# Kernel optimization log

Hardware: AMD Instinct MI355X
Metric: run time of the kernel (lower is better)

Reference implementation:

```python
import jax, jax.numpy as jnp
import numpy as np

B, T, P, D = 8, 512, 2048, 768
TOKEN_HALF = 0.15
PATCH_HALF = 0.03  # small patch boxes


def _make_boxes(key, b, n, half):
    c = jax.random.uniform(key, (b, n, 2), dtype=jnp.float32)
    lo = jnp.clip(c - half, 0.0, 1.0)
    hi = jnp.clip(c + half, 0.0, 1.0)
    return jnp.concatenate([lo, hi], axis=-1)  # (b, n, 4): x0,y0,x1,y1


def setup_inputs() -> dict:
    key = jax.random.key(0)
    k1, k2, k3, k4 = jax.random.split(key, 4)
    patch_feats = jax.random.normal(k1, (B, P, D), dtype=jnp.float32)
    token_boxes = _make_boxes(k2, B, T, TOKEN_HALF)
    patch_boxes = _make_boxes(k3, B, P, PATCH_HALF)
    token_mask = jnp.ones((B, T), dtype=bool)
    scorer_w = jax.random.normal(k4, (D,), dtype=jnp.float32) * 0.02
    scorer_b = jnp.zeros((1,), dtype=jnp.float32)
    return {"patch_feats": patch_feats, "token_boxes": token_boxes,
            "patch_boxes": patch_boxes, "token_mask": token_mask,
            "scorer_w": scorer_w, "scorer_b": scorer_b}


def _patches_in_token_boxes(patch_boxes, tb):
    # patch center containment test: (B,T,P) bool
    cx = 0.5 * (patch_boxes[..., 0] + patch_boxes[..., 2])  # (B,P)
    cy = 0.5 * (patch_boxes[..., 1] + patch_boxes[..., 3])  # (B,P)
    cx = cx[:, None, :]
    cy = cy[:, None, :]
    return ((cx >= tb[..., 0:1]) & (cx <= tb[..., 2:3]) &
            (cy >= tb[..., 1:2]) & (cy <= tb[..., 3:4]))


def reference(patch_feats, token_boxes, patch_boxes, token_mask, scorer_w, scorer_b):
    # normalize token boxes if given in 0..1000 coords (data-dependent, via where)
    tb = token_boxes
    scale = jnp.where(tb.max() > 1.5, jnp.float32(1.0 / 1000.0), jnp.float32(1.0))
    tb = tb * scale

    in_box = _patches_in_token_boxes(patch_boxes, tb)          # (B,T,P)
    in_box = in_box & token_mask[:, :, None]
    region_mask = jnp.any(in_box, axis=-1)                      # (B,T)

    scores = patch_feats @ scorer_w + scorer_b[0]               # (B,P)
    scores = jnp.broadcast_to(scores[:, None, :], in_box.shape)  # (B,T,P)
    scores = jnp.where(in_box, scores, jnp.float32(-10000.0))
    attn = jax.nn.softmax(scores, axis=-1)                      # (B,T,P)

    region_feats = jnp.einsum('btp,bpd->btd', attn, patch_feats)
    region_feats = region_feats * region_mask[..., None].astype(region_feats.dtype)
    return region_feats, region_mask
```

## Files before the change

### kernel.cpp

```cpp
#include <hip/hip_runtime.h>

#define B 8
#define T 512
#define P 2048
#define D 768
#define KDIM P

typedef unsigned short ushort_t;
using short8 = __attribute__((ext_vector_type(8))) short;
using f32x4v = __attribute__((ext_vector_type(4))) float;

#define IDX_SCALE 0
#define IDX_SCORES 64
#define IDX_SCORES2 (64 + B*P)
#define IDX_CX (64 + B*P)
#define IDX_CY (64 + 2*B*P)
#define OFF_ATTN_BYTES 197120
#define OFF_FT_BYTES (OFF_ATTN_BYTES + (size_t)B*T*P*2)
#define WS_NEED (OFF_FT_BYTES + (size_t)B*D*P*2)

#define GLD16(gsrc, ldst) \
    __builtin_amdgcn_global_load_lds((const __attribute__((address_space(1))) void*)(gsrc), \
                                     (__attribute__((address_space(3))) void*)(ldst), 16, 0, 0)

#define SCHED_FENCE() __builtin_amdgcn_sched_barrier(0)
#define RAW_BARRIER() do { SCHED_FENCE(); __builtin_amdgcn_s_barrier(); SCHED_FENCE(); } while (0)

__device__ inline ushort_t f2bf(float x) {
    union { float f; unsigned u; } v; v.f = x;
    unsigned r = v.u + 0x7fffu + ((v.u >> 16) & 1u);
    return (ushort_t)(r >> 16);
}

__global__ void k_scale(const float* __restrict__ tboxes, float* __restrict__ ws) {
    __shared__ float red[4];
    int tid = threadIdx.x;
    float m = -1e30f;
    const float4* tb4 = (const float4*)tboxes;
    #pragma unroll
    for (int i = 0; i < 16; ++i) {
        float4 v = tb4[tid + i * 256];
        m = fmaxf(fmaxf(fmaxf(m, v.x), fmaxf(v.y, v.z)), v.w);
    }
    #pragma unroll
    for (int off = 1; off < 64; off <<= 1) m = fmaxf(m, __shfl_xor(m, off));
    if ((tid & 63) == 0) red[tid >> 6] = m;
    __syncthreads();
    if (tid == 0) {
        float mb = fmaxf(fmaxf(red[0], red[1]), fmaxf(red[2], red[3]));
        ws[IDX_SCALE] = (mb > 1.5f) ? (1.0f / 1000.0f) : 1.0f;
    }
}

__global__ __launch_bounds__(256) void k_prep(const float* __restrict__ feats,
        const float* __restrict__ w, float* __restrict__ ws, ushort_t* __restrict__ fT) {
    __shared__ float tile[2][64][65];
    __shared__ float sred[64][17];
    const int t = threadIdx.x;
    const int p0 = blockIdx.x * 64;
    const int z = blockIdx.y;
    const int b = blockIdx.z;
    const float4* f4 = (const float4*)(feats + ((size_t)b * P + p0) * D);
    const float4* w4 = (const float4*)w;
    const int tr = t >> 4, tc = t & 15;
    float sp[4] = {0.f, 0.f, 0.f, 0.f};

    float4 v[4];
    {
        int dt = z * 6;
        #pragma unroll
        for (int i = 0; i < 4; ++i)
            v[i] = f4[(size_t)(tr + 16 * i) * 192 + dt * 16 + tc];
    }
    int cur = 0;
    for (int it = 0; it < 6; ++it) {
        const int dt = z * 6 + it;
        float4 wv = w4[dt * 16 + tc];
        #pragma unroll
        for (int i = 0; i < 4; ++i) {
            int pr = tr + 16 * i;
            sp[i] += v[i].x * wv.x + v[i].y * wv.y + v[i].z * wv.z + v[i].w * wv.w;
            tile[cur][pr][tc * 4 + 0] = v[i].x;
            tile[cur][pr][tc * 4 + 1] = v[i].y;
            tile[cur][pr][tc * 4 + 2] = v[i].z;
            tile[cur][pr][tc * 4 + 3] = v[i].w;
        }
        __syncthreads();
        if (it < 5) {
            int dt2 = dt + 1;
            #pragma unroll
            for (int i = 0; i < 4; ++i)
                v[i] = f4[(size_t)(tr + 16 * i) * 192 + dt2 * 16 + tc];
        }
        #pragma unroll
        for (int pass = 0; pass < 4; ++pass) {
            int idx = pass * 256 + t;
            int dr = idx >> 4;
            int pq = (idx & 15) * 4;
            unsigned u0 = (unsigned)f2bf(tile[cur][pq + 0][dr]) |
                          ((unsigned)f2bf(tile[cur][pq + 1][dr]) << 16);
            unsigned u1 = (unsigned)f2bf(tile[cur][pq + 2][dr]) |
                          ((unsigned)f2bf(tile[cur][pq + 3][dr]) << 16);
            uint2 o; o.x = u0; o.y = u1;
            *(uint2*)&fT[((size_t)b * D + dt * 64 + dr) * P + p0 + pq] = o;
        }
        cur ^= 1;
    }
    #pragma unroll
    for (int i = 0; i < 4; ++i) sred[tr + 16 * i][tc] = sp[i];
    __syncthreads();
    if (t < 64) {
        float s = 0.f;
        #pragma unroll
        for (int c = 0; c < 16; ++c) s += sred[t][c];
        ws[(z ? IDX_SCORES2 : IDX_SCORES) + b * P + p0 + t] = s;
    }
}

__global__ __launch_bounds__(256) void k_attn(const float* __restrict__ tboxes,
        const float* __restrict__ pboxes, const unsigned char* __restrict__ mask8,
        const float* __restrict__ bias, const float* __restrict__ ws,
        ushort_t* __restrict__ attn, float* __restrict__ out) {
    const int wv = threadIdx.x >> 6;
    const int ln = threadIdx.x & 63;
    const int t = blockIdx.x * 4 + wv;
    const int b = blockIdx.y;
    const int row = b * T + t;
    const float scale = ws[IDX_SCALE];
    const float bs = bias[0];
    const float4 tb = ((const float4*)tboxes)[row];
    const float lox = tb.x * scale, loy = tb.y * scale;
    const float hix = tb.z * scale, hiy = tb.w * scale;
    bool storage_u8 = ((mask8[1] | mask8[2] | mask8[3]) != 0);
    bool tmask = storage_u8 ? (mask8[row] != 0) : (((const int*)mask8)[row] != 0);

    const float2* sA = (const float2*)(ws + IDX_SCORES + b * P);
    const float2* sB = (const float2*)(ws + IDX_SCORES2 + b * P);
    const float4* pb4 = (const float4*)(pboxes + (size_t)b * P * 4);
    unsigned* arow32 = (unsigned*)(attn + (size_t)row * P);

    float s0[16], s1[16];
    float m = -1e30f;
    const float NINF = -__builtin_inff();
    #pragma unroll
    for (int r = 0; r < 16; ++r) {
        int q = ln + 64 * r;
        float2 sa = sA[q], sb = sB[q];
        float v0 = sa.x + sb.x + bs;
        float v1 = sa.y + sb.y + bs;
        float4 b0 = pb4[2 * q], b1 = pb4[2 * q + 1];
        float cx0 = 0.5f * (b0.x + b0.z), cy0 = 0.5f * (b0.y + b0.w);
        float cx1 = 0.5f * (b1.x + b1.z), cy1 = 0.5f * (b1.y + b1.w);
        bool i0 = (cx0 >= lox) && (cx0 <= hix) && (cy0 >= loy) && (cy0 <= hiy);
        bool i1 = (cx1 >= lox) && (cx1 <= hix) && (cy1 >= loy) && (cy1 <= hiy);
        s0[r] = i0 ? v0 : NINF;
        s1[r] = i1 ? v1 : NINF;
        m = fmaxf(m, fmaxf(s0[r], s1[r]));
    }
    #pragma unroll
    for (int off = 1; off < 64; off <<= 1) m = fmaxf(m, __shfl_xor(m, off));
    bool any = m > -1e29f;

    if (!any || !tmask) {
        #pragma unroll
        for (int r = 0; r < 16; ++r) arow32[ln + 64 * r] = 0u;
        if (ln == 0) out[(size_t)B * T * D + row] = 0.f;
        return;
    }
    float lsum = 0.f;
    #pragma unroll
    for (int r = 0; r < 16; ++r) {
        s0[r] = __expf(s0[r] - m);
        s1[r] = __expf(s1[r] - m);
        lsum += s0[r] + s1[r];
    }
    #pragma unroll
    for (int off = 1; off < 64; off <<= 1) lsum += __shfl_xor(lsum, off);
    float invl = 1.0f / lsum;
    #pragma unroll
    for (int r = 0; r < 16; ++r) {
        unsigned lo = (unsigned)f2bf(s0[r] * invl);
        unsigned hi = (unsigned)f2bf(s1[r] * invl);
        arow32[ln + 64 * r] = lo | (hi << 16);
    }
    if (ln == 0) out[(size_t)B * T * D + row] = 1.0f;
}

__global__ __launch_bounds__(256) void k_gemm(const ushort_t* __restrict__ attn,
        const ushort_t* __restrict__ fT, float* __restrict__ out) {
    __shared__ __align__(16) ushort_t As[3 * 8192];
    __shared__ __align__(16) ushort_t Bs[3 * 8192];
    const int tid = threadIdx.x;
    const int lane = tid & 63, wid = tid >> 6;
    const int wm = wid >> 1, wn = wid & 1;

    const int bid = blockIdx.x;
    const int b = bid & 7;
    const int i6 = bid >> 3;
    const int t0 = (i6 & 3) * 128;
    const int n0 = (i6 >> 2) * 128;

    const ushort_t* Ab = attn + ((size_t)b * T + t0) * P;
    const ushort_t* Bb = fT + ((size_t)b * D + n0) * P;

    const int rl8 = lane >> 3;
    const int slot = (lane & 7) ^ rl8;

    f32x4v acc[4][4];
    #pragma unroll
    for (int i = 0; i < 4; ++i)
        #pragma unroll
        for (int j = 0; j < 4; ++j)
            acc[i][j] = (f32x4v){0.f, 0.f, 0.f, 0.f};

    const int lr = lane & 15, hi4 = lane >> 4;

    #define STAGE(buf, kt) do { \
        const ushort_t* a_src = Ab + (size_t)(kt) * 64; \
        const ushort_t* b_src = Bb + (size_t)(kt) * 64; \
        _Pragma("unroll") \
        for (int i = 0; i < 4; ++i) { \
            int c = wid * 4 + i; \
            GLD16(a_src + (size_t)(c * 8 + rl8) * P + slot * 8, &As[(buf) * 8192 + c * 512]); \
        } \
        _Pragma("unroll") \
        for (int i = 0; i < 4; ++i) { \
            int c = wid * 4 + i; \
            GLD16(b_src + (size_t)(c * 8 + rl8) * P + slot * 8, &Bs[(buf) * 8192 + c * 512]); \
        } \
    } while (0)

    #define LDA(row, kslot) (((row) >> 3) * 512 + ((row) & 7) * 64 + (((kslot) ^ ((row) & 7)) * 8))

    #define COMPUTE(buf) do { \
        _Pragma("unroll") \
        for (int ks = 0; ks < 2; ++ks) { \
            short8 a[4], bfr[4]; \
            int kslot = ks * 4 + hi4; \
            _Pragma("unroll") \
            for (int i = 0; i < 4; ++i) \
                a[i] = *(const short8*)&As[(buf) * 8192 + LDA(wm * 64 + i * 16 + lr, kslot)]; \
            _Pragma("unroll") \
            for (int j = 0; j < 4; ++j) \
                bfr[j] = *(const short8*)&Bs[(buf) * 8192 + LDA(wn * 64 + j * 16 + lr, kslot)]; \
            _Pragma("unroll") \
            for (int i = 0; i < 4; ++i) \
                _Pragma("unroll") \
                for (int j = 0; j < 4; ++j) \
                    acc[i][j] = __builtin_amdgcn_mfma_f32_16x16x32_bf16(a[i], bfr[j], acc[i][j], 0, 0, 0); \
        } \
    } while (0)

    STAGE(0, 0);
    STAGE(1, 1);
    int c0 = 0, c2 = 2;
    for (int kt = 0; kt < KDIM / 64 - 2; ++kt) {
        STAGE(c2, kt + 2);
        asm volatile("s_waitcnt vmcnt(16)" ::: "memory");
        RAW_BARRIER();
        COMPUTE(c0);
        RAW_BARRIER();
        c0 = (c0 == 2) ? 0 : c0 + 1;
        c2 = (c2 == 2) ? 0 : c2 + 1;
    }
    asm volatile("s_waitcnt vmcnt(8)" ::: "memory");
    RAW_BARRIER();
    COMPUTE(c0);
    c0 = (c0 == 2) ? 0 : c0 + 1;
    asm volatile("s_waitcnt vmcnt(0)" ::: "memory");
    RAW_BARRIER();
    COMPUTE(c0);

    #pragma unroll
    for (int i = 0; i < 4; ++i) {
        #pragma unroll
        for (int j = 0; j < 4; ++j) {
            int trow = t0 + wm * 64 + i * 16 + hi4 * 4;
            int ncol = n0 + wn * 64 + j * 16 + lr;
            #pragma unroll
            for (int q = 0; q < 4; ++q)
                out[((size_t)(b * T) + trow + q) * D + ncol] = acc[i][j][q];
        }
    }
    #undef STAGE
    #undef LDA
    #undef COMPUTE
}

__global__ __launch_bounds__(256) void k_scores_fb(
        const float* __restrict__ feats, const float* __restrict__ pboxes,
        const float* __restrict__ w, const float* __restrict__ bias,
        float* __restrict__ ws) {
    int row = blockIdx.x * 4 + (threadIdx.x >> 6);
    int lane = threadIdx.x & 63;
    const float* f = feats + (size_t)row * D;
    float acc = 0.f;
    #pragma unroll
    for (int k = 0; k < D / 64; ++k) acc += f[lane + k * 64] * w[lane + k * 64];
    #pragma unroll
    for (int off = 1; off < 64; off <<= 1) acc += __shfl_xor(acc, off);
    if (lane == 0) {
        ws[IDX_SCORES + row] = acc + bias[0];
        ws[IDX_CX + row] = 0.5f * (pboxes[row * 4 + 0] + pboxes[row * 4 + 2]);
        ws[IDX_CY + row] = 0.5f * (pboxes[row * 4 + 1] + pboxes[row * 4 + 3]);
    }
}

__global__ __launch_bounds__(256) void k_main_fb(
        const float* __restrict__ feats, const float* __restrict__ tboxes,
        const unsigned char* __restrict__ mask8,
        const float* __restrict__ ws, float* __restrict__ out) {
    const int t = blockIdx.x, b = blockIdx.y;
    const int tid = threadIdx.x;
    const float scale = ws[IDX_SCALE];
    const float* scores = ws + IDX_SCORES;
    const float* cxs = ws + IDX_CX;
    const float* cys = ws + IDX_CY;
    const int row = b * T + t;
    const float lo_x = tboxes[row * 4 + 0] * scale;
    const float lo_y = tboxes[row * 4 + 1] * scale;
    const float hi_x = tboxes[row * 4 + 2] * scale;
    const float hi_y = tboxes[row * 4 + 3] * scale;
    bool storage_u8 = ((mask8[1] | mask8[2] | mask8[3]) != 0);
    bool tmask = storage_u8 ? (mask8[row] != 0) : (((const int*)mask8)[row] != 0);
    float s[8]; bool ib[8];
    float m = -1e30f;
    #pragma unroll
    for (int j = 0; j < 8; ++j) {
        int p = tid + j * 256;
        float cx = cxs[b * P + p], cy = cys[b * P + p];
        bool in = (cx >= lo_x) && (cx <= hi_x) && (cy >= lo_y) && (cy <= hi_y);
        ib[j] = in;
        s[j] = scores[b * P + p];
        if (in) m = fmaxf(m, s[j]);
    }
    __shared__ float s_red[4];
    #pragma unroll
    for (int off = 1; off < 64; off <<= 1) m = fmaxf(m, __shfl_xor(m, off));
    if ((tid & 63) == 0) s_red[tid >> 6] = m;
    __syncthreads();
    float mb = fmaxf(fmaxf(s_red[0], s_red[1]), fmaxf(s_red[2], s_red[3]));
    bool any = mb > -1e29f;
    const size_t obase = (size_t)row * D;
    if (!any || !tmask) {
        out[obase + tid] = 0.f; out[obase + tid + 256] = 0.f; out[obase + tid + 512] = 0.f;
        if (tid == 0) out[(size_t)B * T * D + row] = 0.f;
        return;
    }
    float w8[8]; int c = 0; float lsum = 0.f;
    #pragma unroll
    for (int j = 0; j < 8; ++j) {
        float wv = ib[j] ? __expf(s[j] - mb) : 0.f;
        w8[j] = wv; lsum += wv;
        if (ib[j]) ++c;
    }
    __shared__ float s_sum[4];
    #pragma unroll
    for (int off = 1; off < 64; off <<= 1) lsum += __shfl_xor(lsum, off);
    if ((tid & 63) == 0) s_sum[tid >> 6] = lsum;
    __syncthreads();
    float l = s_sum[0] + s_sum[1] + s_sum[2] + s_sum[3];
    __shared__ int s_cnt[256];
    s_cnt[tid] = c;
    __syncthreads();
    #pragma unroll
    for (int off = 1; off < 256; off <<= 1) {
        int v = (tid >= off) ? s_cnt[tid - off] : 0;
        __syncthreads();
        s_cnt[tid] += v;
        __syncthreads();
    }
    int excl = s_cnt[tid] - c;
    int nnz = s_cnt[255];
    __shared__ int s_idx[P];
    __shared__ float s_wt[P];
    int o = excl;
    #pragma unroll
    for (int j = 0; j < 8; ++j) {
        if (ib[j]) { s_idx[o] = tid + j * 256; s_wt[o] = w8[j]; ++o; }
    }
    __syncthreads();
    float a0 = 0.f, a1 = 0.f, a2 = 0.f;
    const float* fb = feats + (size_t)b * P * D;
    for (int i = 0; i < nnz; ++i) {
        int p = s_idx[i];
        float wv = s_wt[i];
        const float* fr = fb + (size_t)p * D + tid;
        a0 += wv * fr[0]; a1 += wv * fr[256]; a2 += wv * fr[512];
    }
    float inv = 1.0f / l;
    out[obase + tid] = a0 * inv;
    out[obase + tid + 256] = a1 * inv;
    out[obase + tid + 512] = a2 * inv;
    if (tid == 0) out[(size_t)B * T * D + row] = 1.0f;
}

extern "C" void kernel_launch(void* const* d_in, const int* in_sizes, int n_in,
                              void* d_out, int out_size, void* d_ws, size_t ws_size,
                              hipStream_t stream) {
    const float* feats  = (const float*)d_in[0];
    const float* tboxes = (const float*)d_in[1];
    const float* pboxes = (const float*)d_in[2];
    const unsigned char* tmask = (const unsigned char*)d_in[3];
    const float* w      = (const float*)d_in[4];
    const float* bias   = (const float*)d_in[5];
    float* out = (float*)d_out;
    float* ws  = (float*)d_ws;

    if (ws_size >= WS_NEED) {
        ushort_t* attn = (ushort_t*)((char*)d_ws + OFF_ATTN_BYTES);
        ushort_t* fT   = (ushort_t*)((char*)d_ws + OFF_FT_BYTES);
        k_scale<<<1, 256, 0, stream>>>(tboxes, ws);
        k_prep<<<dim3(P / 64, 2, B), 256, 0, stream>>>(feats, w, ws, fT);
        k_attn<<<dim3(T / 4, B), 256, 0, stream>>>(tboxes, pboxes, tmask, bias, ws, attn, out);
        k_gemm<<<dim3((T / 128) * (D / 128) * B), 256, 0, stream>>>(attn, fT, out);
    } else {
        k_scale<<<1, 256, 0, stream>>>(tboxes, ws);
        k_scores_fb<<<(B * P) / 4, 256, 0, stream>>>(feats, pboxes, w, bias, ws);
        k_main_fb<<<dim3(T, B), 256, 0, stream>>>(feats, tboxes, tmask, ws, out);
    }
}
```

Measured before the change: 70.04 us.

## Split GEMM K dimension four ways with partial buffers and a reduce kernel

```diff
diff --git a/kernel.cpp b/kernel.cpp
--- a/kernel.cpp
+++ b/kernel.cpp
@@ -5,6 +5,8 @@
 #define P 2048
 #define D 768
 #define KDIM P
+#define NSPLIT 4
+#define KSPLIT (KDIM / NSPLIT)
 
 typedef unsigned short ushort_t;
 using short8 = __attribute__((ext_vector_type(8))) short;
@@ -17,14 +19,12 @@
 #define IDX_CY (64 + 2*B*P)
 #define OFF_ATTN_BYTES 197120
 #define OFF_FT_BYTES (OFF_ATTN_BYTES + (size_t)B*T*P*2)
-#define WS_NEED (OFF_FT_BYTES + (size_t)B*D*P*2)
+#define OFF_PART_BYTES (OFF_FT_BYTES + (size_t)B*D*P*2)
+#define WS_NEED (OFF_PART_BYTES + (size_t)NSPLIT*B*T*D*4)
 
 #define GLD16(gsrc, ldst) \
     __builtin_amdgcn_global_load_lds((const __attribute__((address_space(1))) void*)(gsrc), \
                                      (__attribute__((address_space(3))) void*)(ldst), 16, 0, 0)
-
-#define SCHED_FENCE() __builtin_amdgcn_sched_barrier(0)
-#define RAW_BARRIER() do { SCHED_FENCE(); __builtin_amdgcn_s_barrier(); SCHED_FENCE(); } while (0)
 
 __device__ inline ushort_t f2bf(float x) {
     union { float f; unsigned u; } v; v.f = x;
@@ -186,22 +186,25 @@
     if (ln == 0) out[(size_t)B * T * D + row] = 1.0f;
 }
 
-__global__ __launch_bounds__(256) void k_gemm(const ushort_t* __restrict__ attn,
-        const ushort_t* __restrict__ fT, float* __restrict__ out) {
-    __shared__ __align__(16) ushort_t As[3 * 8192];
-    __shared__ __align__(16) ushort_t Bs[3 * 8192];
+__global__ __launch_bounds__(256, 3) void k_gemm(const ushort_t* __restrict__ attn,
+        const ushort_t* __restrict__ fT, float* __restrict__ partial) {
+    __shared__ __align__(16) ushort_t As[8192];
+    __shared__ __align__(16) ushort_t Bs[8192];
     const int tid = threadIdx.x;
     const int lane = tid & 63, wid = tid >> 6;
     const int wm = wid >> 1, wn = wid & 1;
 
     const int bid = blockIdx.x;
     const int b = bid & 7;
-    const int i6 = bid >> 3;
-    const int t0 = (i6 & 3) * 128;
-    const int n0 = (i6 >> 2) * 128;
-
-    const ushort_t* Ab = attn + ((size_t)b * T + t0) * P;
-    const ushort_t* Bb = fT + ((size_t)b * D + n0) * P;
+    const int w = bid >> 3;
+    const int s = w / 24;
+    const int tile = w % 24;
+    const int t0 = (tile & 3) * 128;
+    const int n0 = (tile >> 2) * 128;
+    const int kbase = s * KSPLIT;
+
+    const ushort_t* Ab = attn + ((size_t)b * T + t0) * P + kbase;
+    const ushort_t* Bb = fT + ((size_t)b * D + n0) * P + kbase;
 
     const int rl8 = lane >> 3;
     const int slot = (lane & 7) ^ rl8;
@@ -215,62 +218,43 @@
 
     const int lr = lane & 15, hi4 = lane >> 4;
 
-    #define STAGE(buf, kt) do { \
-        const ushort_t* a_src = Ab + (size_t)(kt) * 64; \
-        const ushort_t* b_src = Bb + (size_t)(kt) * 64; \
-        _Pragma("unroll") \
-        for (int i = 0; i < 4; ++i) { \
-            int c = wid * 4 + i; \
-            GLD16(a_src + (size_t)(c * 8 + rl8) * P + slot * 8, &As[(buf) * 8192 + c * 512]); \
-        } \
-        _Pragma("unroll") \
-        for (int i = 0; i < 4; ++i) { \
-            int c = wid * 4 + i; \
-            GLD16(b_src + (size_t)(c * 8 + rl8) * P + slot * 8, &Bs[(buf) * 8192 + c * 512]); \
-        } \
-    } while (0)
-
     #define LDA(row, kslot) (((row) >> 3) * 512 + ((row) & 7) * 64 + (((kslot) ^ ((row) & 7)) * 8))
 
-    #define COMPUTE(buf) do { \
-        _Pragma("unroll") \
-        for (int ks = 0; ks < 2; ++ks) { \
-            short8 a[4], bfr[4]; \
-            int kslot = ks * 4 + hi4; \
-            _Pragma("unroll") \
-            for (int i = 0; i < 4; ++i) \
-                a[i] = *(const short8*)&As[(buf) * 8192 + LDA(wm * 64 + i * 16 + lr, kslot)]; \
-            _Pragma("unroll") \
-            for (int j = 0; j < 4; ++j) \
-                bfr[j] = *(const short8*)&Bs[(buf) * 8192 + LDA(wn * 64 + j * 16 + lr, kslot)]; \
-            _Pragma("unroll") \
-            for (int i = 0; i < 4; ++i) \
-                _Pragma("unroll") \
-                for (int j = 0; j < 4; ++j) \
-                    acc[i][j] = __builtin_amdgcn_mfma_f32_16x16x32_bf16(a[i], bfr[j], acc[i][j], 0, 0, 0); \
-        } \
-    } while (0)
-
-    STAGE(0, 0);
-    STAGE(1, 1);
-    int c0 = 0, c2 = 2;
-    for (int kt = 0; kt < KDIM / 64 - 2; ++kt) {
-        STAGE(c2, kt + 2);
-        asm volatile("s_waitcnt vmcnt(16)" ::: "memory");
-        RAW_BARRIER();
-        COMPUTE(c0);
-        RAW_BARRIER();
-        c0 = (c0 == 2) ? 0 : c0 + 1;
-        c2 = (c2 == 2) ? 0 : c2 + 1;
-    }
-    asm volatile("s_waitcnt vmcnt(8)" ::: "memory");
-    RAW_BARRIER();
-    COMPUTE(c0);
-    c0 = (c0 == 2) ? 0 : c0 + 1;
-    asm volatile("s_waitcnt vmcnt(0)" ::: "memory");
-    RAW_BARRIER();
-    COMPUTE(c0);
-
+    for (int kt = 0; kt < KSPLIT / 64; ++kt) {
+        const ushort_t* a_src = Ab + (size_t)kt * 64;
+        const ushort_t* b_src = Bb + (size_t)kt * 64;
+        #pragma unroll
+        for (int i = 0; i < 4; ++i) {
+            int c = wid * 4 + i;
+            GLD16(a_src + (size_t)(c * 8 + rl8) * P + slot * 8, &As[c * 512]);
+        }
+        #pragma unroll
+        for (int i = 0; i < 4; ++i) {
+            int c = wid * 4 + i;
+            GLD16(b_src + (size_t)(c * 8 + rl8) * P + slot * 8, &Bs[c * 512]);
+        }
+        __syncthreads();
+        #pragma unroll
+        for (int ks = 0; ks < 2; ++ks) {
+            short8 a[4], bfr[4];
+            int kslot = ks * 4 + hi4;
+            #pragma unroll
+            for (int i = 0; i < 4; ++i)
+                a[i] = *(const short8*)&As[LDA(wm * 64 + i * 16 + lr, kslot)];
+            #pragma unroll
+            for (int j = 0; j < 4; ++j)
+                bfr[j] = *(const short8*)&Bs[LDA(wn * 64 + j * 16 + lr, kslot)];
+            #pragma unroll
+            for (int i = 0; i < 4; ++i)
+                #pragma unroll
+                for (int j = 0; j < 4; ++j)
+                    acc[i][j] = __builtin_amdgcn_mfma_f32_16x16x32_bf16(a[i], bfr[j], acc[i][j], 0, 0, 0);
+        }
+        __syncthreads();
+    }
+    #undef LDA
+
+    float* pout = partial + (size_t)s * B * T * D;
     #pragma unroll
     for (int i = 0; i < 4; ++i) {
         #pragma unroll
@@ -279,12 +263,23 @@
             int ncol = n0 + wn * 64 + j * 16 + lr;
             #pragma unroll
             for (int q = 0; q < 4; ++q)
-                out[((size_t)(b * T) + trow + q) * D + ncol] = acc[i][j][q];
-        }
-    }
-    #undef STAGE
-    #undef LDA
-    #undef COMPUTE
+                pout[((size_t)(b * T) + trow + q) * D + ncol] = acc[i][j][q];
+        }
+    }
+}
+
+__global__ __launch_bounds__(256) void k_reduce(const float* __restrict__ partial,
+                                                float* __restrict__ out) {
+    const size_t i = (size_t)blockIdx.x * 256 + threadIdx.x;
+    const size_t stride = (size_t)(B * T * D) / 4;
+    const float4* p = (const float4*)partial;
+    float4 a = p[i], b2 = p[i + stride], c = p[i + 2 * stride], d = p[i + 3 * stride];
+    float4 r;
+    r.x = ((a.x + b2.x) + c.x) + d.x;
+    r.y = ((a.y + b2.y) + c.y) + d.y;
+    r.z = ((a.z + b2.z) + c.z) + d.z;
+    r.w = ((a.w + b2.w) + c.w) + d.w;
+    ((float4*)out)[i] = r;
 }
 
 __global__ __launch_bounds__(256) void k_scores_fb(
@@ -410,10 +405,12 @@
     if (ws_size >= WS_NEED) {
         ushort_t* attn = (ushort_t*)((char*)d_ws + OFF_ATTN_BYTES);
         ushort_t* fT   = (ushort_t*)((char*)d_ws + OFF_FT_BYTES);
+        float* part    = (float*)((char*)d_ws + OFF_PART_BYTES);
         k_scale<<<1, 256, 0, stream>>>(tboxes, ws);
         k_prep<<<dim3(P / 64, 2, B), 256, 0, stream>>>(feats, w, ws, fT);
         k_attn<<<dim3(T / 4, B), 256, 0, stream>>>(tboxes, pboxes, tmask, bias, ws, attn, out);
-        k_gemm<<<dim3((T / 128) * (D / 128) * B), 256, 0, stream>>>(attn, fT, out);
+        k_gemm<<<dim3(NSPLIT * B * (T / 128) * (D / 128)), 256, 0, stream>>>(attn, fT, part);
+        k_reduce<<<dim3(B * T * D / 4 / 256), 256, 0, stream>>>(part, out);
     } else {
         k_scale<<<1, 256, 0, stream>>>(tboxes, ws);
         k_scores_fb<<<(B * P) / 4, 256, 0, stream>>>(feats, pboxes, w, bias, ws);
```

Result: faster. 62.66 us (-10.5%).

## Split GEMM K dimension into two sequential launches with accumulate epilogue

Applied to the files above, without the earlier changes.

```diff
diff --git a/kernel.cpp b/kernel.cpp
--- a/kernel.cpp
+++ b/kernel.cpp
@@ -5,6 +5,7 @@
 #define P 2048
 #define D 768
 #define KDIM P
+#define KHALF (KDIM / 2)
 
 typedef unsigned short ushort_t;
 using short8 = __attribute__((ext_vector_type(8))) short;
@@ -186,22 +187,23 @@
     if (ln == 0) out[(size_t)B * T * D + row] = 1.0f;
 }
 
+template <int ACC>
 __global__ __launch_bounds__(256) void k_gemm(const ushort_t* __restrict__ attn,
-        const ushort_t* __restrict__ fT, float* __restrict__ out) {
-    __shared__ __align__(16) ushort_t As[3 * 8192];
-    __shared__ __align__(16) ushort_t Bs[3 * 8192];
+        const ushort_t* __restrict__ fT, float* __restrict__ out, int kbase) {
+    __shared__ __align__(16) ushort_t As[2 * 8192];
+    __shared__ __align__(16) ushort_t Bs[2 * 8192];
     const int tid = threadIdx.x;
     const int lane = tid & 63, wid = tid >> 6;
     const int wm = wid >> 1, wn = wid & 1;
 
     const int bid = blockIdx.x;
     const int b = bid & 7;
-    const int i6 = bid >> 3;
-    const int t0 = (i6 & 3) * 128;
-    const int n0 = (i6 >> 2) * 128;
-
-    const ushort_t* Ab = attn + ((size_t)b * T + t0) * P;
-    const ushort_t* Bb = fT + ((size_t)b * D + n0) * P;
+    const int rem = bid >> 3;
+    const int t0 = (rem & 3) * 128;
+    const int n0 = (rem >> 2) * 128;
+
+    const ushort_t* Ab = attn + ((size_t)b * T + t0) * P + kbase;
+    const ushort_t* Bb = fT + ((size_t)b * D + n0) * P + kbase;
 
     const int rl8 = lane >> 3;
     const int slot = (lane & 7) ^ rl8;
@@ -252,24 +254,18 @@
     } while (0)
 
     STAGE(0, 0);
-    STAGE(1, 1);
-    int c0 = 0, c2 = 2;
-    for (int kt = 0; kt < KDIM / 64 - 2; ++kt) {
-        STAGE(c2, kt + 2);
-        asm volatile("s_waitcnt vmcnt(16)" ::: "memory");
+    int cur = 0;
+    for (int kt = 0; kt < KHALF / 64 - 1; ++kt) {
+        STAGE(cur ^ 1, kt + 1);
+        asm volatile("s_waitcnt vmcnt(8)" ::: "memory");
         RAW_BARRIER();
-        COMPUTE(c0);
+        COMPUTE(cur);
         RAW_BARRIER();
-        c0 = (c0 == 2) ? 0 : c0 + 1;
-        c2 = (c2 == 2) ? 0 : c2 + 1;
-    }
-    asm volatile("s_waitcnt vmcnt(8)" ::: "memory");
-    RAW_BARRIER();
-    COMPUTE(c0);
-    c0 = (c0 == 2) ? 0 : c0 + 1;
+        cur ^= 1;
+    }
     asm volatile("s_waitcnt vmcnt(0)" ::: "memory");
     RAW_BARRIER();
-    COMPUTE(c0);
+    COMPUTE(cur);
 
     #pragma unroll
     for (int i = 0; i < 4; ++i) {
@@ -278,8 +274,11 @@
             int trow = t0 + wm * 64 + i * 16 + hi4 * 4;
             int ncol = n0 + wn * 64 + j * 16 + lr;
             #pragma unroll
-            for (int q = 0; q < 4; ++q)
-                out[((size_t)(b * T) + trow + q) * D + ncol] = acc[i][j][q];
+            for (int q = 0; q < 4; ++q) {
+                size_t idx = ((size_t)(b * T) + trow + q) * D + ncol;
+                if (ACC) out[idx] += acc[i][j][q];
+                else     out[idx]  = acc[i][j][q];
+            }
         }
     }
     #undef STAGE
@@ -413,7 +412,8 @@
         k_scale<<<1, 256, 0, stream>>>(tboxes, ws);
         k_prep<<<dim3(P / 64, 2, B), 256, 0, stream>>>(feats, w, ws, fT);
         k_attn<<<dim3(T / 4, B), 256, 0, stream>>>(tboxes, pboxes, tmask, bias, ws, attn, out);
-        k_gemm<<<dim3((T / 128) * (D / 128) * B), 256, 0, stream>>>(attn, fT, out);
+        k_gemm<0><<<dim3(B * (T / 128) * (D / 128)), 256, 0, stream>>>(attn, fT, out, 0);
+        k_gemm<1><<<dim3(B * (T / 128) * (D / 128)), 256, 0, stream>>>(attn, fT, out, KHALF);
     } else {
         k_scale<<<1, 256, 0, stream>>>(tboxes, ws);
         k_scores_fb<<<(B * P) / 4, 256, 0, stream>>>(feats, pboxes, w, bias, ws);
```

Measured after the change: 77.07 us. +10.0%, slower.
